# Kernel tuning notes

Measured on AMD Instinct MI355X. Metric: run time of the kernel, lower is better.

Reference implementation:

```python
import jax, jax.numpy as jnp
import numpy as np

DIL = (1, 2, 4, 8)  # dilations, num_dilation = 4
KS = 3              # kernel_size
EPS = 1e-5


def _unfold3(x, r):
    """nn.Unfold(3, dilation=r, padding=r): x [B,d,H,W] -> [B,d,9,H*W]."""
    B, d, H, W = x.shape
    xp = jnp.pad(x, ((0, 0), (0, 0), (r, r), (r, r)))
    cols = jnp.stack([xp[:, :, i * r:i * r + H, j * r:j * r + W]
                      for i in range(KS) for j in range(KS)], axis=2)
    return cols.reshape(B, d, KS * KS, H * W)


def setup_inputs() -> dict:
    key = jax.random.key(0)
    ks = jax.random.split(key, 8)
    B, C, H, W = 8, 256, 80, 80
    s = 0.05
    return {
        "x": jax.random.normal(ks[0], (B, C, H, W), jnp.float32),
        "qkv_w": jax.random.normal(ks[1], (3 * C, C), jnp.float32) * s,
        "qkv_b": jnp.zeros((3 * C,), jnp.float32),
        "fc_w": jax.random.normal(ks[2], (4, 4), jnp.float32) * 0.3,
        "fc_b": jnp.zeros((4,), jnp.float32),
        "ln_g": jnp.ones((C // 4,), jnp.float32),
        "ln_b": jnp.zeros((C // 4,), jnp.float32),
        "proj_w": jax.random.normal(ks[3], (C, C), jnp.float32) * s,
        "proj_b": jnp.zeros((C,), jnp.float32),
        "w1": jax.random.normal(ks[4], (2 * C, C), jnp.float32) * s,
        "bn1_g": jnp.ones((2 * C,), jnp.float32),
        "bn1_b": jnp.zeros((2 * C,), jnp.float32),
        "bn1_m": jnp.zeros((2 * C,), jnp.float32),
        "bn1_v": jnp.ones((2 * C,), jnp.float32),
        "w2": jax.random.normal(ks[5], (C, 2 * C), jnp.float32) * s,
        "bn2_g": jnp.ones((C,), jnp.float32),
        "bn2_b": jnp.zeros((C,), jnp.float32),
        "bn2_m": jnp.zeros((C,), jnp.float32),
        "bn2_v": jnp.ones((C,), jnp.float32),
    }


def _bn(z, g, b, m, v):
    # BatchNorm2d, eval mode (running stats), z is [B,C,H,W]
    inv = g / jnp.sqrt(v + EPS)
    return z * inv[None, :, None, None] + (b - m * inv)[None, :, None, None]


def _psablock(x, qkv_w, qkv_b, fc_w, fc_b, ln_g, ln_b, proj_w, proj_b,
              w1, bn1_g, bn1_b, bn1_m, bn1_v, w2, bn2_g, bn2_b, bn2_m, bn2_v):
    B, C, H, W = x.shape
    ND = len(DIL)
    Cd = C // ND                  # channels per dilation branch
    num_heads = 4
    hd = C // num_heads           # head_dim = 64
    nh = Cd // hd                 # heads per branch (= 1)
    scale = hd ** -0.5

    # qkv 1x1 conv: [B,3C,H,W] -> (3, ND, Cd) split
    qkv = jnp.einsum('bchw,oc->bohw', x, qkv_w) + qkv_b[None, :, None, None]
    qkv = qkv.reshape(B, 3, ND, Cd, H, W)

    feats = []
    for i, r in enumerate(DIL):
        q, k, v = qkv[:, 0, i], qkv[:, 1, i], qkv[:, 2, i]
        qh = q.reshape(B, nh, hd, H * W)                       # [B,nh,hd,N]
        kh = _unfold3(k, r).reshape(B, nh, hd, KS * KS, H * W)  # [B,nh,hd,9,N]
        vh = _unfold3(v, r).reshape(B, nh, hd, KS * KS, H * W)
        attn = jax.nn.softmax(
            jnp.einsum('bhcn,bhcjn->bhnj', qh, kh) * scale, axis=-1)
        out = jnp.einsum('bhnj,bhcjn->bnhc', attn, vh)          # [B,N,nh,hd]
        feats.append(out.reshape(B, H, W, Cd))

    # CrossScaleFusion: Linear over scale dim + residual + LayerNorm over Cd
    stacked = jnp.stack(feats, axis=3)                          # [B,H,W,S,Cd]
    fused = jnp.einsum('bhwsc,ts->bhwtc', stacked, fc_w) \
        + fc_b[None, None, None, :, None]
    fused = fused + stacked
    mu = fused.mean(-1, keepdims=True)
    var = fused.var(-1, keepdims=True)
    normed = (fused - mu) / jnp.sqrt(var + EPS) * ln_g + ln_b

    y2 = normed.reshape(B, H, W, C)
    y3 = jnp.einsum('bhwc,oc->bhwo', y2, proj_w) + proj_b
    attn_out = y3.transpose(0, 3, 1, 2)                         # [B,C,H,W]

    x1 = x + attn_out                                           # shortcut

    # FFN: Conv1x1(C->2C)+BN+SiLU, Conv1x1(2C->C)+BN, residual
    h = jnp.einsum('bchw,oc->bohw', x1, w1)
    h = jax.nn.silu(_bn(h, bn1_g, bn1_b, bn1_m, bn1_v))
    h = jnp.einsum('bchw,oc->bohw', h, w2)
    h = _bn(h, bn2_g, bn2_b, bn2_m, bn2_v)
    return x1 + h


def reference(x, qkv_w, qkv_b, fc_w, fc_b, ln_g, ln_b, proj_w, proj_b,
              w1, bn1_g, bn1_b, bn1_m, bn1_v, w2, bn2_g, bn2_b, bn2_m, bn2_v):
    return _psablock(x, qkv_w, qkv_b, fc_w, fc_b, ln_g, ln_b, proj_w, proj_b,
                     w1, bn1_g, bn1_b, bn1_m, bn1_v,
                     w2, bn2_g, bn2_b, bn2_m, bn2_v)
```

## Files before the change

### kernel.cpp

```cpp
#include <hip/hip_runtime.h>

#define EPS_F 1e-5f

typedef __attribute__((ext_vector_type(8))) short short8;
typedef __attribute__((ext_vector_type(4))) float f32x4;
typedef __attribute__((ext_vector_type(4))) unsigned short ushort4v;
typedef __attribute__((address_space(1))) void gvoid;
typedef __attribute__((address_space(3))) void svoid;

__device__ __forceinline__ float bf2f(unsigned short u){
    union { unsigned int i; float f; } v; v.i = ((unsigned int)u) << 16; return v.f;
}
__device__ __forceinline__ unsigned short f2bf(float f){
    union { float f; unsigned int i; } v; v.f = f;
    unsigned int r = v.i + 0x7FFFu + ((v.i >> 16) & 1u);
    return (unsigned short)(r >> 16);
}

template<int EPI>
__global__ __launch_bounds__(256, 2)
void mm_k(const short* __restrict__ A, const short* __restrict__ Bt,
          const int M, const int K,
          const float* __restrict__ p0, const float* __restrict__ p1,
          const float* __restrict__ p2, const float* __restrict__ p3,
          const float* __restrict__ resid,
          short* __restrict__ outT, float* __restrict__ outF)
{
    const int N = 6400;
    __shared__ short lsA[128 * 64];
    __shared__ short lsB[128 * 64];

    const int b  = blockIdx.z;
    const int n0 = blockIdx.x * 128;
    const int m0 = blockIdx.y * 128;
    const int t  = threadIdx.x;
    const int l  = t & 63;
    const int w  = t >> 6;
    const int wr = w >> 1, wc = w & 1;

    const short* Bb = Bt + (size_t)b * N * K;

    f32x4 acc[4][4];
    #pragma unroll
    for (int i = 0; i < 4; ++i)
        #pragma unroll
        for (int j = 0; j < 4; ++j) acc[i][j] = (f32x4){0.f, 0.f, 0.f, 0.f};

    const int rsub = l >> 3;
    const int csub = l & 7;

    for (int k0 = 0; k0 < K; k0 += 64) {
        #pragma unroll
        for (int q = 0; q < 4; ++q) {
            const int row = (w * 4 + q) * 8 + rsub;
            const int cs  = csub ^ (row & 7);
            const short* ga = A  + (size_t)(m0 + row) * K + k0 + (cs << 3);
            __builtin_amdgcn_global_load_lds((gvoid*)ga, (svoid*)(lsA + (w * 4 + q) * 512), 16, 0, 0);
            const short* gb = Bb + (size_t)(n0 + row) * K + k0 + (cs << 3);
            __builtin_amdgcn_global_load_lds((gvoid*)gb, (svoid*)(lsB + (w * 4 + q) * 512), 16, 0, 0);
        }
        __syncthreads();

        #pragma unroll
        for (int ks = 0; ks < 2; ++ks) {
            short8 av[4], bv[4];
            const int cfr = ks * 4 + (l >> 4);
            #pragma unroll
            for (int mi = 0; mi < 4; ++mi) {
                const int row = wr * 64 + mi * 16 + (l & 15);
                av[mi] = *(const short8*)&lsA[row * 64 + ((cfr ^ (row & 7)) << 3)];
            }
            #pragma unroll
            for (int ni = 0; ni < 4; ++ni) {
                const int row = wc * 64 + ni * 16 + (l & 15);
                bv[ni] = *(const short8*)&lsB[row * 64 + ((cfr ^ (row & 7)) << 3)];
            }
            #pragma unroll
            for (int mi = 0; mi < 4; ++mi)
                #pragma unroll
                for (int ni = 0; ni < 4; ++ni)
                    acc[mi][ni] = __builtin_amdgcn_mfma_f32_16x16x32_bf16(
                        av[mi], bv[ni], acc[mi][ni], 0, 0, 0);
        }
        __syncthreads();
    }

    const int mq = (l >> 4) * 4;
    const int nq = l & 15;
    #pragma unroll
    for (int mi = 0; mi < 4; ++mi) {
        const int mb = m0 + wr * 64 + mi * 16 + mq;
        float mul[4], add[4];
        #pragma unroll
        for (int j = 0; j < 4; ++j) {
            const int m = mb + j;
            if (EPI == 0 || EPI == 1) { mul[j] = 1.f; add[j] = p0[m]; }
            else { const float inv = p0[m] * rsqrtf(p3[m] + EPS_F);
                   mul[j] = inv; add[j] = p1[m] - p2[m] * inv; }
        }
        #pragma unroll
        for (int ni = 0; ni < 4; ++ni) {
            const int n = n0 + wc * 64 + ni * 16 + nq;
            float z[4];
            #pragma unroll
            for (int j = 0; j < 4; ++j) {
                z[j] = acc[mi][ni][j] * mul[j] + add[j];
                if (EPI == 2) z[j] = z[j] / (1.f + __expf(-z[j]));
                if (EPI == 1 || EPI == 3)
                    z[j] += resid[((size_t)b * M + mb + j) * N + n];
            }
            if (EPI == 0 || EPI == 1 || EPI == 2) {
                ushort4v u;
                #pragma unroll
                for (int j = 0; j < 4; ++j) u[j] = f2bf(z[j]);
                *(ushort4v*)&outT[((size_t)b * N + n) * M + mb] = u;
            }
            if (EPI == 1 || EPI == 3) {
                #pragma unroll
                for (int j = 0; j < 4; ++j)
                    outF[((size_t)b * M + mb + j) * N + n] = z[j];
            }
        }
    }
}

__global__ __launch_bounds__(256, 2)
void attn_k(const short* __restrict__ qkvt,
            const float* __restrict__ fc_w, const float* __restrict__ fc_b,
            const float* __restrict__ ln_g, const float* __restrict__ ln_b,
            short* __restrict__ y2t)
{
    __shared__ float st[4][64][64];

    const int b   = blockIdx.y;
    const int hw0 = blockIdx.x * 64;
    const int t   = threadIdx.x;
    const int di  = t >> 6;
    const int px  = t & 63;
    const int hw  = hw0 + px;
    const int yy  = hw / 80;
    const int xx  = hw % 80;
    const int r   = 1 << di;

    int  off[9];
    bool ok[9];
    #pragma unroll
    for (int jy = 0; jy < 3; ++jy)
        #pragma unroll
        for (int jx = 0; jx < 3; ++jx) {
            const int ny = yy + (jy - 1) * r;
            const int nx = xx + (jx - 1) * r;
            const bool o = (ny >= 0) && (ny < 80) && (nx >= 0) && (nx < 80);
            ok[jy * 3 + jx]  = o;
            off[jy * 3 + jx] = o ? (ny * 80 + nx) : 0;
        }

    const short* qp = qkvt + ((size_t)b * 6400 + hw) * 768 + di * 64;
    float qf[64];
    #pragma unroll
    for (int c8 = 0; c8 < 8; ++c8) {
        const short8 v = *(const short8*)&qp[c8 * 8];
        #pragma unroll
        for (int u = 0; u < 8; ++u) qf[c8 * 8 + u] = bf2f((unsigned short)v[u]);
    }

    float s[9];
    #pragma unroll
    for (int j = 0; j < 9; ++j) s[j] = 0.f;
    #pragma unroll
    for (int j = 0; j < 9; ++j) if (ok[j]) {
        const short* kp = qkvt + ((size_t)b * 6400 + off[j]) * 768 + 256 + di * 64;
        float a = 0.f;
        #pragma unroll
        for (int c8 = 0; c8 < 8; ++c8) {
            const short8 kv = *(const short8*)&kp[c8 * 8];
            #pragma unroll
            for (int u = 0; u < 8; ++u)
                a = fmaf(qf[c8 * 8 + u], bf2f((unsigned short)kv[u]), a);
        }
        s[j] = a;
    }

    const float scale = 0.125f;
    float mx = s[0] * scale;
    #pragma unroll
    for (int j = 1; j < 9; ++j) mx = fmaxf(mx, s[j] * scale);
    float e[9], sum = 0.f;
    #pragma unroll
    for (int j = 0; j < 9; ++j) { e[j] = __expf(s[j] * scale - mx); sum += e[j]; }
    const float isum = 1.f / sum;

    #pragma unroll
    for (int c8 = 0; c8 < 8; ++c8) {
        float o[8];
        #pragma unroll
        for (int u = 0; u < 8; ++u) o[u] = 0.f;
        #pragma unroll
        for (int j = 0; j < 9; ++j) if (ok[j]) {
            const short* vp = qkvt + ((size_t)b * 6400 + off[j]) * 768 + 512 + di * 64;
            const short8 vv = *(const short8*)&vp[c8 * 8];
            #pragma unroll
            for (int u = 0; u < 8; ++u)
                o[u] = fmaf(e[j], bf2f((unsigned short)vv[u]), o[u]);
        }
        #pragma unroll
        for (int u = 0; u < 8; ++u) st[di][c8 * 8 + u][px] = o[u] * isum;
    }
    __syncthreads();

    float fwv[4];
    #pragma unroll
    for (int s4 = 0; s4 < 4; ++s4) fwv[s4] = fc_w[di * 4 + s4];
    const float fb = fc_b[di];

    float f[64], mu = 0.f;
    #pragma unroll
    for (int c = 0; c < 64; ++c) {
        float v = fb + st[di][c][px];
        #pragma unroll
        for (int s4 = 0; s4 < 4; ++s4) v = fmaf(fwv[s4], st[s4][c][px], v);
        f[c] = v; mu += v;
    }
    mu *= (1.f / 64.f);
    float var = 0.f;
    #pragma unroll
    for (int c = 0; c < 64; ++c) { const float d = f[c] - mu; var = fmaf(d, d, var); }
    var *= (1.f / 64.f);
    const float rstd = rsqrtf(var + EPS_F);

    short* yo = y2t + ((size_t)b * 6400 + hw) * 256 + di * 64;
    #pragma unroll
    for (int c8 = 0; c8 < 8; ++c8) {
        short8 v;
        #pragma unroll
        for (int u = 0; u < 8; ++u) {
            const int c = c8 * 8 + u;
            v[u] = (short)f2bf((f[c] - mu) * rstd * ln_g[c] + ln_b[c]);
        }
        *(short8*)&yo[c8 * 8] = v;
    }
}

__global__ void xt_k(const float* __restrict__ x, short* __restrict__ xt)
{
    const int b  = blockIdx.y;
    const int hw = blockIdx.x * 256 + threadIdx.x;
    const float* xb = x + (size_t)b * 256 * 6400 + hw;
    short* o = xt + ((size_t)b * 6400 + hw) * 256;
    #pragma unroll 4
    for (int c8 = 0; c8 < 32; ++c8) {
        short8 v;
        #pragma unroll
        for (int u = 0; u < 8; ++u)
            v[u] = (short)f2bf(xb[(size_t)(c8 * 8 + u) * 6400]);
        *(short8*)&o[c8 * 8] = v;
    }
}

__global__ void wc_k(const float* __restrict__ a, const float* __restrict__ bb,
                     const float* __restrict__ c, const float* __restrict__ d,
                     short* __restrict__ o)
{
    const int i = blockIdx.x * 256 + threadIdx.x;
    float v;
    if      (i < 196608)  v = a[i];
    else if (i < 262144)  v = bb[i - 196608];
    else if (i < 393216)  v = c[i - 262144];
    else                  v = d[i - 393216];
    o[i] = (short)f2bf(v);
}

extern "C" void kernel_launch(void* const* d_in, const int* in_sizes, int n_in,
                              void* d_out, int out_size, void* d_ws, size_t ws_size,
                              hipStream_t stream)
{
    const float* x      = (const float*)d_in[0];
    const float* qkv_w  = (const float*)d_in[1];
    const float* qkv_b  = (const float*)d_in[2];
    const float* fc_w   = (const float*)d_in[3];
    const float* fc_b   = (const float*)d_in[4];
    const float* ln_g   = (const float*)d_in[5];
    const float* ln_b   = (const float*)d_in[6];
    const float* proj_w = (const float*)d_in[7];
    const float* proj_b = (const float*)d_in[8];
    const float* w1     = (const float*)d_in[9];
    const float* bn1_g  = (const float*)d_in[10];
    const float* bn1_b  = (const float*)d_in[11];
    const float* bn1_m  = (const float*)d_in[12];
    const float* bn1_v  = (const float*)d_in[13];
    const float* w2     = (const float*)d_in[14];
    const float* bn2_g  = (const float*)d_in[15];
    const float* bn2_b  = (const float*)d_in[16];
    const float* bn2_m  = (const float*)d_in[17];
    const float* bn2_v  = (const float*)d_in[18];
    float* out = (float*)d_out;

    const int B = 8, HW = 6400;

    char* ws = (char*)d_ws;
    short* wqkvb = (short*)(ws + 0);
    short* wprojb = wqkvb + 196608;
    short* w1b    = wprojb + 65536;
    short* w2b    = w1b + 131072;
    short* xt     = (short*)(ws + 1048576);
    short* qkvt   = (short*)(ws + 27262976);
    short* y2t    = (short*)(ws + 105906176);
    short* x1t    = (short*)(ws + 132120576);
    float* x1f    = (float*)(ws + 158334976);
    short* h      = qkvt;

    dim3 blk(256);

    wc_k<<<dim3(2048), blk, 0, stream>>>(qkv_w, proj_w, w1, w2, wqkvb);

    xt_k<<<dim3(25, B), blk, 0, stream>>>(x, xt);

    mm_k<0><<<dim3(50, 6, B), blk, 0, stream>>>(
        wqkvb, xt, 768, 256, qkv_b, nullptr, nullptr, nullptr, nullptr,
        qkvt, nullptr);

    attn_k<<<dim3(100, B), blk, 0, stream>>>(qkvt, fc_w, fc_b, ln_g, ln_b, y2t);

    mm_k<1><<<dim3(50, 2, B), blk, 0, stream>>>(
        wprojb, y2t, 256, 256, proj_b, nullptr, nullptr, nullptr, x,
        x1t, x1f);

    mm_k<2><<<dim3(50, 4, B), blk, 0, stream>>>(
        w1b, x1t, 512, 256, bn1_g, bn1_b, bn1_m, bn1_v, nullptr,
        h, nullptr);

    mm_k<3><<<dim3(50, 2, B), blk, 0, stream>>>(
        w2b, h, 256, 512, bn2_g, bn2_b, bn2_m, bn2_v, x1f,
        nullptr, out);
}
```

Baseline: 458.2 us.

## Rework attention kernel registers, LDS layout and flatten grids with batch-interleaved block order

The attention kernel stops holding 64 q floats and 64 fused values per thread. It streams q in chunks of 8 against all nine keys, stores the per-branch outputs as swizzled bf16 rows in LDS, computes the LayerNorm mean and variance in one pass, and recomputes the fused values instead of keeping them. Out-of-bounds neighbours become masked loads of a valid address rather than branches, and launch bounds are raised to four blocks per CU. All grids are flattened with the batch index in the low bits, which changes the order blocks are scheduled in and may improve L2 reuse of weight tiles. The trade-offs are an extra bf16 rounding of the attention output before the fc/LN step, a one-pass variance that is less numerically stable, and wasted loads for masked neighbours.

```diff
diff --git a/kernel.cpp b/kernel.cpp
--- a/kernel.cpp
+++ b/kernel.cpp
@@ -30,9 +30,11 @@
     __shared__ short lsA[128 * 64];
     __shared__ short lsB[128 * 64];
 
-    const int b  = blockIdx.z;
-    const int n0 = blockIdx.x * 128;
-    const int m0 = blockIdx.y * 128;
+    const int id = blockIdx.x;
+    const int b  = id & 7;
+    const int rr = id >> 3;
+    const int n0 = (rr % 50) * 128;
+    const int m0 = (rr / 50) * 128;
     const int t  = threadIdx.x;
     const int l  = t & 63;
     const int w  = t >> 6;
@@ -124,16 +126,17 @@
     }
 }
 
-__global__ __launch_bounds__(256, 2)
+__global__ __launch_bounds__(256, 4)
 void attn_k(const short* __restrict__ qkvt,
             const float* __restrict__ fc_w, const float* __restrict__ fc_b,
             const float* __restrict__ ln_g, const float* __restrict__ ln_b,
             short* __restrict__ y2t)
 {
-    __shared__ float st[4][64][64];
-
-    const int b   = blockIdx.y;
-    const int hw0 = blockIdx.x * 64;
+    __shared__ short st[4][64][64];
+
+    const int id  = blockIdx.x;
+    const int b   = id & 7;
+    const int hw0 = (id >> 3) * 64;
     const int t   = threadIdx.x;
     const int di  = t >> 6;
     const int px  = t & 63;
@@ -142,8 +145,8 @@
     const int xx  = hw % 80;
     const int r   = 1 << di;
 
-    int  off[9];
-    bool ok[9];
+    int   off[9];
+    float okf[9];
     #pragma unroll
     for (int jy = 0; jy < 3; ++jy)
         #pragma unroll
@@ -151,44 +154,43 @@
             const int ny = yy + (jy - 1) * r;
             const int nx = xx + (jx - 1) * r;
             const bool o = (ny >= 0) && (ny < 80) && (nx >= 0) && (nx < 80);
-            ok[jy * 3 + jx]  = o;
-            off[jy * 3 + jx] = o ? (ny * 80 + nx) : 0;
-        }
-
-    const short* qp = qkvt + ((size_t)b * 6400 + hw) * 768 + di * 64;
-    float qf[64];
+            okf[jy * 3 + jx] = o ? 1.f : 0.f;
+            off[jy * 3 + jx] = o ? (ny * 80 + nx) : hw;
+        }
+
+    const short* qp = qkvt + ((size_t)(b * 6400 + hw)) * 768 + di * 64;
+
+    float s[9];
+    #pragma unroll
+    for (int j = 0; j < 9; ++j) s[j] = 0.f;
     #pragma unroll
     for (int c8 = 0; c8 < 8; ++c8) {
-        const short8 v = *(const short8*)&qp[c8 * 8];
-        #pragma unroll
-        for (int u = 0; u < 8; ++u) qf[c8 * 8 + u] = bf2f((unsigned short)v[u]);
-    }
-
-    float s[9];
-    #pragma unroll
-    for (int j = 0; j < 9; ++j) s[j] = 0.f;
-    #pragma unroll
-    for (int j = 0; j < 9; ++j) if (ok[j]) {
-        const short* kp = qkvt + ((size_t)b * 6400 + off[j]) * 768 + 256 + di * 64;
-        float a = 0.f;
-        #pragma unroll
-        for (int c8 = 0; c8 < 8; ++c8) {
-            const short8 kv = *(const short8*)&kp[c8 * 8];
+        const short8 qv = *(const short8*)&qp[c8 * 8];
+        float qf[8];
+        #pragma unroll
+        for (int u = 0; u < 8; ++u) qf[u] = bf2f((unsigned short)qv[u]);
+        #pragma unroll
+        for (int j = 0; j < 9; ++j) {
+            const short8 kv = *(const short8*)(qkvt +
+                ((size_t)(b * 6400 + off[j])) * 768 + 256 + di * 64 + c8 * 8);
             #pragma unroll
             for (int u = 0; u < 8; ++u)
-                a = fmaf(qf[c8 * 8 + u], bf2f((unsigned short)kv[u]), a);
-        }
-        s[j] = a;
-    }
-
-    const float scale = 0.125f;
-    float mx = s[0] * scale;
-    #pragma unroll
-    for (int j = 1; j < 9; ++j) mx = fmaxf(mx, s[j] * scale);
+                s[j] = fmaf(qf[u], bf2f((unsigned short)kv[u]), s[j]);
+        }
+    }
+    #pragma unroll
+    for (int j = 0; j < 9; ++j) s[j] *= okf[j] * 0.125f;
+
+    float mx = s[0];
+    #pragma unroll
+    for (int j = 1; j < 9; ++j) mx = fmaxf(mx, s[j]);
     float e[9], sum = 0.f;
     #pragma unroll
-    for (int j = 0; j < 9; ++j) { e[j] = __expf(s[j] * scale - mx); sum += e[j]; }
+    for (int j = 0; j < 9; ++j) { e[j] = __expf(s[j] - mx); sum += e[j]; }
     const float isum = 1.f / sum;
+    float pe[9];
+    #pragma unroll
+    for (int j = 0; j < 9; ++j) pe[j] = e[j] * isum * okf[j];
 
     #pragma unroll
     for (int c8 = 0; c8 < 8; ++c8) {
@@ -196,48 +198,67 @@
         #pragma unroll
         for (int u = 0; u < 8; ++u) o[u] = 0.f;
         #pragma unroll
-        for (int j = 0; j < 9; ++j) if (ok[j]) {
-            const short* vp = qkvt + ((size_t)b * 6400 + off[j]) * 768 + 512 + di * 64;
-            const short8 vv = *(const short8*)&vp[c8 * 8];
+        for (int j = 0; j < 9; ++j) {
+            const short8 vv = *(const short8*)(qkvt +
+                ((size_t)(b * 6400 + off[j])) * 768 + 512 + di * 64 + c8 * 8);
             #pragma unroll
             for (int u = 0; u < 8; ++u)
-                o[u] = fmaf(e[j], bf2f((unsigned short)vv[u]), o[u]);
-        }
-        #pragma unroll
-        for (int u = 0; u < 8; ++u) st[di][c8 * 8 + u][px] = o[u] * isum;
+                o[u] = fmaf(pe[j], bf2f((unsigned short)vv[u]), o[u]);
+        }
+        short8 ov;
+        #pragma unroll
+        for (int u = 0; u < 8; ++u) ov[u] = (short)f2bf(o[u]);
+        *(short8*)&st[di][px][(c8 ^ (px & 7)) << 3] = ov;
     }
     __syncthreads();
 
-    float fwv[4];
-    #pragma unroll
-    for (int s4 = 0; s4 < 4; ++s4) fwv[s4] = fc_w[di * 4 + s4];
+    float cw[4];
+    #pragma unroll
+    for (int s4 = 0; s4 < 4; ++s4) cw[s4] = fc_w[di * 4 + s4] + (s4 == di ? 1.f : 0.f);
     const float fb = fc_b[di];
 
-    float f[64], mu = 0.f;
-    #pragma unroll
-    for (int c = 0; c < 64; ++c) {
-        float v = fb + st[di][c][px];
-        #pragma unroll
-        for (int s4 = 0; s4 < 4; ++s4) v = fmaf(fwv[s4], st[s4][c][px], v);
-        f[c] = v; mu += v;
+    float mu = 0.f, sq = 0.f;
+    #pragma unroll
+    for (int c8 = 0; c8 < 8; ++c8) {
+        const int cc = (c8 ^ (px & 7)) << 3;
+        const short8 a0 = *(const short8*)&st[0][px][cc];
+        const short8 a1 = *(const short8*)&st[1][px][cc];
+        const short8 a2 = *(const short8*)&st[2][px][cc];
+        const short8 a3 = *(const short8*)&st[3][px][cc];
+        #pragma unroll
+        for (int u = 0; u < 8; ++u) {
+            float f = fb;
+            f = fmaf(cw[0], bf2f((unsigned short)a0[u]), f);
+            f = fmaf(cw[1], bf2f((unsigned short)a1[u]), f);
+            f = fmaf(cw[2], bf2f((unsigned short)a2[u]), f);
+            f = fmaf(cw[3], bf2f((unsigned short)a3[u]), f);
+            mu += f; sq = fmaf(f, f, sq);
+        }
     }
     mu *= (1.f / 64.f);
-    float var = 0.f;
-    #pragma unroll
-    for (int c = 0; c < 64; ++c) { const float d = f[c] - mu; var = fmaf(d, d, var); }
-    var *= (1.f / 64.f);
+    const float var  = sq * (1.f / 64.f) - mu * mu;
     const float rstd = rsqrtf(var + EPS_F);
 
-    short* yo = y2t + ((size_t)b * 6400 + hw) * 256 + di * 64;
+    short* yo = y2t + ((size_t)(b * 6400 + hw)) * 256 + di * 64;
     #pragma unroll
     for (int c8 = 0; c8 < 8; ++c8) {
-        short8 v;
+        const int cc = (c8 ^ (px & 7)) << 3;
+        const short8 a0 = *(const short8*)&st[0][px][cc];
+        const short8 a1 = *(const short8*)&st[1][px][cc];
+        const short8 a2 = *(const short8*)&st[2][px][cc];
+        const short8 a3 = *(const short8*)&st[3][px][cc];
+        short8 ov;
         #pragma unroll
         for (int u = 0; u < 8; ++u) {
+            float f = fb;
+            f = fmaf(cw[0], bf2f((unsigned short)a0[u]), f);
+            f = fmaf(cw[1], bf2f((unsigned short)a1[u]), f);
+            f = fmaf(cw[2], bf2f((unsigned short)a2[u]), f);
+            f = fmaf(cw[3], bf2f((unsigned short)a3[u]), f);
             const int c = c8 * 8 + u;
-            v[u] = (short)f2bf((f[c] - mu) * rstd * ln_g[c] + ln_b[c]);
-        }
-        *(short8*)&yo[c8 * 8] = v;
+            ov[u] = (short)f2bf((f - mu) * rstd * ln_g[c] + ln_b[c]);
+        }
+        *(short8*)&yo[c8 * 8] = ov;
     }
 }
 
@@ -295,10 +316,10 @@
     const float* bn2_v  = (const float*)d_in[18];
     float* out = (float*)d_out;
 
-    const int B = 8, HW = 6400;
+    const int B = 8;
 
     char* ws = (char*)d_ws;
-    short* wqkvb = (short*)(ws + 0);
+    short* wqkvb  = (short*)(ws + 0);
     short* wprojb = wqkvb + 196608;
     short* w1b    = wprojb + 65536;
     short* w2b    = w1b + 131072;
@@ -315,21 +336,21 @@
 
     xt_k<<<dim3(25, B), blk, 0, stream>>>(x, xt);
 
-    mm_k<0><<<dim3(50, 6, B), blk, 0, stream>>>(
+    mm_k<0><<<dim3(50 * 6 * 8), blk, 0, stream>>>(
         wqkvb, xt, 768, 256, qkv_b, nullptr, nullptr, nullptr, nullptr,
         qkvt, nullptr);
 
-    attn_k<<<dim3(100, B), blk, 0, stream>>>(qkvt, fc_w, fc_b, ln_g, ln_b, y2t);
-
-    mm_k<1><<<dim3(50, 2, B), blk, 0, stream>>>(
+    attn_k<<<dim3(800), blk, 0, stream>>>(qkvt, fc_w, fc_b, ln_g, ln_b, y2t);
+
+    mm_k<1><<<dim3(50 * 2 * 8), blk, 0, stream>>>(
         wprojb, y2t, 256, 256, proj_b, nullptr, nullptr, nullptr, x,
         x1t, x1f);
 
-    mm_k<2><<<dim3(50, 4, B), blk, 0, stream>>>(
+    mm_k<2><<<dim3(50 * 4 * 8), blk, 0, stream>>>(
         w1b, x1t, 512, 256, bn1_g, bn1_b, bn1_m, bn1_v, nullptr,
         h, nullptr);
 
-    mm_k<3><<<dim3(50, 2, B), blk, 0, stream>>>(
+    mm_k<3><<<dim3(50 * 2 * 8), blk, 0, stream>>>(
         w2b, h, 256, 512, bn2_g, bn2_b, bn2_m, bn2_v, x1f,
         nullptr, out);
 }
```

Measured after the change: 439.8 us. 4.0% less time.
